# Kernel optimization log

Hardware: AMD Instinct MI355X
Metric: run time of the kernel (lower is better)

The kernel has to match this reference:

```python
import jax, jax.numpy as jnp
import numpy as np

# Gating config (matches init_kwargs)
N_GROUPS = 4        # n_expert_groups
TOPK_GROUPS = 2     # n_limited_groups
TOPK = 4            # n_activated_experts
ROUTE_SCALE = 1.0


def setup_inputs() -> dict:
    key = jax.random.key(0)
    ks = jax.random.split(key, 8)
    T, D, E, I = 2048, 1024, 16, 512
    s = 0.02  # init scale for sane numerics
    return {
        "x": jax.random.normal(ks[0], (T, D), jnp.float32),
        "gate_w": jax.random.normal(ks[1], (E, D), jnp.float32) * s,
        "w1": jax.random.normal(ks[2], (E, I, D), jnp.float32) * s,
        "w2": jax.random.normal(ks[3], (E, D, I), jnp.float32) * s,
        "w3": jax.random.normal(ks[4], (E, I, D), jnp.float32) * s,
        "ws1": jax.random.normal(ks[5], (I, D), jnp.float32) * s,
        "ws2": jax.random.normal(ks[6], (D, I), jnp.float32) * s,
        "ws3": jax.random.normal(ks[7], (I, D), jnp.float32) * s,
    }


def _gate(x, gate_w):
    # GateDeepSeekV3.forward: softmax scores, group-limited routing, top-k experts.
    T = x.shape[0]
    scores = jax.nn.softmax((x @ gate_w.T).astype(jnp.float32), axis=-1)  # [T, E]
    original_scores = scores
    E = scores.shape[-1]
    # group-limited routing: keep top `TOPK_GROUPS` groups by max score (bias is None)
    s = scores.reshape(T, N_GROUPS, E // N_GROUPS)
    group_scores = s.max(axis=-1)                                  # [T, G]
    _, gidx = jax.lax.top_k(group_scores, TOPK_GROUPS)             # [T, Gk]
    mask = jnp.zeros((T, N_GROUPS), scores.dtype).at[jnp.arange(T)[:, None], gidx].set(1.0)
    s = (s * mask[:, :, None]).reshape(T, E)
    _, indices = jax.lax.top_k(s, TOPK)                            # [T, topk]
    weights = jnp.take_along_axis(original_scores, indices, axis=1) * ROUTE_SCALE
    return weights.astype(x.dtype), indices


def reference(x, gate_w, w1, w2, w3, ws1, ws2, ws3):
    T, D = x.shape
    E = w1.shape[0]
    weights, indices = _gate(x, gate_w)
    # dense [T, E] combine weights (topk indices are unique per token)
    gate_dense = jnp.zeros((T, E), x.dtype).at[jnp.arange(T)[:, None], indices].add(weights)
    # routed experts: y_t = sum_e g[t,e] * W2_e (silu(W1_e x) * (W3_e x))
    h = jax.nn.silu(jnp.einsum('td,eid->tei', x, w1)) * jnp.einsum('td,eid->tei', x, w3)
    y = jnp.einsum('tei,te,edi->td', h, gate_dense, w2)
    # shared expert MLP over all tokens
    z = (jax.nn.silu(x @ ws1.T) * (x @ ws3.T)) @ ws2.T
    return y + z
```

## Files before the change

### kernel.cpp

```cpp
#include <hip/hip_runtime.h>
#include <hip/hip_bf16.h>
#include <math.h>

typedef float v4f __attribute__((ext_vector_type(4)));
typedef short v8s __attribute__((ext_vector_type(8)));

#define T_TOK   2048
#define DDIM    1024
#define NE      16
#define IDIM    512
#define S_ROUTED 8192
#define S_ALL   10240
#define MAXTILE 104

#define OFF_TOPKI    0u
#define OFF_TOPKW    32768u
#define OFF_PART     65536u
#define OFF_CBASE    69632u
#define OFF_SEGOFF   73728u
#define OFF_NTILES   74240u
#define OFF_TROW     74752u
#define OFF_TEND     75776u
#define OFF_TEXP     76800u
#define OFF_SLOTWT   81920u
#define OFF_S2T      114688u
#define OFF_SLOTOF   155648u
#define OFF_XBF      (1u<<20)
#define OFF_H        (8u<<20)
#define OFF_YP       (24u<<20)

__device__ __forceinline__ unsigned short f2bf(float f) {
    unsigned int u = __float_as_uint(f);
    unsigned int r = (u + 0x7fffu + ((u >> 16) & 1u)) >> 16;
    return (unsigned short)r;
}
__device__ __forceinline__ float bf2f(unsigned short s) {
    return __uint_as_float((unsigned)s << 16);
}

#define GLL16(gp, lp) __builtin_amdgcn_global_load_lds( \
    (__attribute__((address_space(1))) void*)(gp), \
    (__attribute__((address_space(3))) void*)(lp), 16, 0, 0)

__global__ __launch_bounds__(256) void gate_kernel(
    const float* __restrict__ x, const float* __restrict__ gw,
    int* __restrict__ topki, float* __restrict__ topkw,
    unsigned short* __restrict__ xbf)
{
    int t = blockIdx.x;
    int tid = threadIdx.x, lane = tid & 63, wave = tid >> 6;
    const float4* xr = (const float4*)(x + (size_t)t * DDIM);
    float4 xv[4];
#pragma unroll
    for (int j = 0; j < 4; j++) xv[j] = xr[lane + 64 * j];

    __shared__ float sc[NE];
#pragma unroll
    for (int ee = 0; ee < 4; ee++) {
        int e = wave * 4 + ee;
        const float4* wr = (const float4*)(gw + (size_t)e * DDIM);
        float acc = 0.f;
#pragma unroll
        for (int j = 0; j < 4; j++) {
            float4 w = wr[lane + 64 * j];
            acc += xv[j].x * w.x + xv[j].y * w.y + xv[j].z * w.z + xv[j].w * w.w;
        }
#pragma unroll
        for (int off = 32; off; off >>= 1) acc += __shfl_down(acc, off, 64);
        if (lane == 0) sc[e] = acc;
    }
    if (wave == 0) {
#pragma unroll
        for (int j = 0; j < 4; j++) {
            int base = 4 * (lane + 64 * j);
            uint2 p;
            p.x = (unsigned)f2bf(xv[j].x) | ((unsigned)f2bf(xv[j].y) << 16);
            p.y = (unsigned)f2bf(xv[j].z) | ((unsigned)f2bf(xv[j].w) << 16);
            *(uint2*)(xbf + (size_t)t * DDIM + base) = p;
        }
    }
    __syncthreads();
    if (tid == 0) {
        float mx = sc[0];
#pragma unroll
        for (int e = 1; e < NE; e++) mx = fmaxf(mx, sc[e]);
        float sco[NE]; float sum = 0.f;
#pragma unroll
        for (int e = 0; e < NE; e++) { sco[e] = __expf(sc[e] - mx); sum += sco[e]; }
        float inv = 1.f / sum;
#pragma unroll
        for (int e = 0; e < NE; e++) sco[e] *= inv;
        float gs[4];
#pragma unroll
        for (int g = 0; g < 4; g++) {
            float m = sco[4 * g];
            m = fmaxf(m, sco[4 * g + 1]); m = fmaxf(m, sco[4 * g + 2]); m = fmaxf(m, sco[4 * g + 3]);
            gs[g] = m;
        }
        int g0 = 0;
        for (int g = 1; g < 4; g++) if (gs[g] > gs[g0]) g0 = g;
        int g1 = -1;
        for (int g = 0; g < 4; g++) { if (g == g0) continue; if (g1 < 0 || gs[g] > gs[g1]) g1 = g; }
        float ms[NE];
#pragma unroll
        for (int e = 0; e < NE; e++) {
            int g = e >> 2;
            ms[e] = (g == g0 || g == g1) ? sco[e] : 0.0f;
        }
        bool used[NE] = {false};
        for (int k = 0; k < 4; k++) {
            int best = -1;
            for (int e = 0; e < NE; e++) {
                if (used[e]) continue;
                if (best < 0 || ms[e] > ms[best]) best = e;
            }
            used[best] = true;
            topki[t * 4 + k] = best;
            topkw[t * 4 + k] = sco[best];
        }
    }
}

__global__ __launch_bounds__(256) void hist_kernel(
    const int* __restrict__ topki, int* __restrict__ part)
{
    __shared__ int cnt[16];
    int tid = threadIdx.x, b = blockIdx.x;
    if (tid < 16) cnt[tid] = 0;
    __syncthreads();
    int e = topki[b * 256 + tid];
    int lane = tid & 63;
#pragma unroll
    for (int e0 = 0; e0 < 16; e0++) {
        unsigned long long mask = __ballot(e == e0);
        if (lane == 0) atomicAdd(&cnt[e0], __popcll(mask));
    }
    __syncthreads();
    if (tid < 16) part[b * 16 + tid] = cnt[tid];
}

__global__ __launch_bounds__(256) void scan_kernel(
    const int* __restrict__ part, int* __restrict__ cbase, int* __restrict__ segoff,
    int* __restrict__ trow, int* __restrict__ tend, int* __restrict__ texp,
    int* __restrict__ ntp)
{
    int tid = threadIdx.x;
    __shared__ int tot[16];
    __shared__ int so[17];
    if (tid < 16) {
        int s = 0;
        for (int b = 0; b < 32; b++) s += part[b * 16 + tid];
        tot[tid] = s;
    }
    __syncthreads();
    if (tid == 0) {
        int off = 0;
        for (int e = 0; e < 16; e++) { so[e] = off; segoff[e] = off; off += tot[e]; }
        so[16] = off; segoff[16] = off; segoff[17] = off + T_TOK;
        int nt = 0;
        for (int e = 0; e < 17; e++) {
            int n = (e < 16) ? tot[e] : T_TOK;
            int base = (e < 16) ? so[e] : S_ROUTED;
            for (int m = 0; m < n; m += 128) {
                trow[nt] = base + m; tend[nt] = base + n; texp[nt] = e; nt++;
            }
        }
        *ntp = nt;
    }
    __syncthreads();
    if (tid < 16) {
        int run = so[tid];
        for (int b = 0; b < 32; b++) { cbase[b * 16 + tid] = run; run += part[b * 16 + tid]; }
    }
}

__global__ __launch_bounds__(256) void assign_kernel(
    const int* __restrict__ topki, const float* __restrict__ topkw,
    const int* __restrict__ cbase, int* __restrict__ s2t,
    float* __restrict__ slotwt, int* __restrict__ slotof)
{
    int b = blockIdx.x, tid = threadIdx.x;
    int i = b * 256 + tid;
    int e = topki[i];
    int lane = tid & 63, wave = tid >> 6;
    __shared__ int wcnt[4][16];
    int lrank = 0;
#pragma unroll
    for (int e0 = 0; e0 < 16; e0++) {
        unsigned long long mask = __ballot(e == e0);
        if (e == e0) lrank = __popcll(mask & ((1ull << lane) - 1ull));
        if (lane == 0) wcnt[wave][e0] = __popcll(mask);
    }
    __syncthreads();
    int pre = 0;
    for (int w = 0; w < wave; w++) pre += wcnt[w][e];
    int slot = cbase[b * 16 + e] + pre + lrank;
    int t = i >> 2;
    s2t[slot] = t;
    slotwt[slot] = topkw[i];
    slotof[i] = slot;
    if ((i & 3) == 0) s2t[S_ROUTED + t] = t;
}

__global__ __launch_bounds__(256, 3) void gemm1_kernel(
    const float* __restrict__ w1, const float* __restrict__ w3,
    const float* __restrict__ s1, const float* __restrict__ s3,
    const unsigned short* __restrict__ xbf,
    unsigned short* __restrict__ h, const float* __restrict__ slotwt,
    const int* __restrict__ s2t,
    const int* __restrict__ trow, const int* __restrict__ tend,
    const int* __restrict__ texp, const int* __restrict__ ntp)
{
    int bid = blockIdx.x;
    int tile = bid >> 3, ct = bid & 7;
    if (tile >= *ntp) return;
    int row0 = trow[tile], rend = tend[tile], e = texp[tile];
    int n0 = ct * 64;
    const float* B1 = (e < 16) ? (w1 + (size_t)e * 524288) : s1;
    const float* B3 = (e < 16) ? (w3 + (size_t)e * 524288) : s3;

    __shared__ __align__(16) short As[128 * 64];
    __shared__ __align__(16) short Bs[128 * 64];

    int tid = threadIdx.x;
    int lane = tid & 63, wave = tid >> 6;
    int wm = wave & 1, wn = wave >> 1;
    int mq = lane >> 4, nl = lane & 15;
    int rr = lane >> 3, cbl = (lane & 7) ^ rr;

    int tok[4];
#pragma unroll
    for (int j = 0; j < 4; j++)
        tok[j] = s2t[row0 + wave * 32 + j * 8 + rr];

    const float* bsrc[4];
    int brow[4], bblk[4];
#pragma unroll
    for (int j = 0; j < 4; j++) {
        int u = tid + 256 * j;
        brow[j] = u >> 3; bblk[j] = u & 7;
        int half = brow[j] >> 6;
        const float* base = half ? B3 : B1;
        bsrc[j] = base + (size_t)(n0 + (brow[j] & 63)) * DDIM + bblk[j] * 8;
    }

    v4f acc[4][4];
#pragma unroll
    for (int i = 0; i < 4; i++)
#pragma unroll
        for (int j = 0; j < 4; j++) acc[i][j] = (v4f)0.f;

    float4 br0[4], br1[4];
#pragma unroll
    for (int j = 0; j < 4; j++) {
        br0[j] = *(const float4*)(bsrc[j]);
        br1[j] = *(const float4*)(bsrc[j] + 4);
    }

    for (int ki = 0; ki < 16; ki++) {
        int kc = ki * 64;
        __syncthreads();
#pragma unroll
        for (int j = 0; j < 4; j++)
            GLL16(xbf + (size_t)tok[j] * DDIM + kc + cbl * 8, As + wave * 2048 + j * 512);
#pragma unroll
        for (int j = 0; j < 4; j++) {
            uint4 p;
            p.x = (unsigned)f2bf(br0[j].x) | ((unsigned)f2bf(br0[j].y) << 16);
            p.y = (unsigned)f2bf(br0[j].z) | ((unsigned)f2bf(br0[j].w) << 16);
            p.z = (unsigned)f2bf(br1[j].x) | ((unsigned)f2bf(br1[j].y) << 16);
            p.w = (unsigned)f2bf(br1[j].z) | ((unsigned)f2bf(br1[j].w) << 16);
            *(uint4*)(Bs + brow[j] * 64 + ((bblk[j] ^ (brow[j] & 7)) * 8)) = p;
        }
        __syncthreads();
        if (ki < 15) {
#pragma unroll
            for (int j = 0; j < 4; j++) {
                br0[j] = *(const float4*)(bsrc[j] + kc + 64);
                br1[j] = *(const float4*)(bsrc[j] + kc + 68);
            }
        }
#pragma unroll
        for (int ks = 0; ks < 2; ks++) {
            int kb = ks * 4 + mq;
            v8s a[4], b[4];
#pragma unroll
            for (int mi = 0; mi < 4; mi++) {
                int R = wm * 64 + mi * 16 + nl;
                a[mi] = *(const v8s*)(As + R * 64 + ((kb ^ (nl & 7)) * 8));
            }
#pragma unroll
            for (int ni = 0; ni < 4; ni++) {
                int S = (ni >> 1) * 64 + wn * 32 + (ni & 1) * 16 + nl;
                b[ni] = *(const v8s*)(Bs + S * 64 + ((kb ^ (nl & 7)) * 8));
            }
#pragma unroll
            for (int mi = 0; mi < 4; mi++)
#pragma unroll
                for (int ni = 0; ni < 4; ni++)
                    acc[mi][ni] = __builtin_amdgcn_mfma_f32_16x16x32_bf16(a[mi], b[ni], acc[mi][ni], 0, 0, 0);
        }
    }
#pragma unroll
    for (int mi = 0; mi < 4; mi++) {
#pragma unroll
        for (int r = 0; r < 4; r++) {
            int srow = row0 + wm * 64 + mi * 16 + mq * 4 + r;
            if (srow < rend) {
                float g = (srow < S_ROUTED) ? slotwt[srow] : 1.0f;
#pragma unroll
                for (int ni = 0; ni < 2; ni++) {
                    float p1 = acc[mi][ni][r], p3 = acc[mi][ni + 2][r];
                    float sig = 1.f / (1.f + __expf(-p1));
                    h[(size_t)srow * IDIM + n0 + wn * 32 + ni * 16 + nl] = f2bf(p1 * sig * p3 * g);
                }
            }
        }
    }
}

__global__ __launch_bounds__(256, 3) void gemm2_kernel(
    const float* __restrict__ w2, const float* __restrict__ s2w,
    const unsigned short* __restrict__ h, unsigned short* __restrict__ yp,
    const int* __restrict__ trow, const int* __restrict__ tend,
    const int* __restrict__ texp, const int* __restrict__ ntp)
{
    int bid = blockIdx.x;
    int tile = bid >> 3, ct = bid & 7;
    if (tile >= *ntp) return;
    int row0 = trow[tile], rend = tend[tile], e = texp[tile];
    int n0 = ct * 128;
    const float* B = ((e < 16) ? (w2 + (size_t)e * 524288) : s2w) + (size_t)n0 * IDIM;

    __shared__ __align__(16) short As[128 * 64];
    __shared__ __align__(16) short Bs[128 * 64];

    int tid = threadIdx.x;
    int lane = tid & 63, wave = tid >> 6;
    int wm = wave & 1, wn = wave >> 1;
    int mq = lane >> 4, nl = lane & 15;
    int rr = lane >> 3, cbl = (lane & 7) ^ rr;

    const float* bsrc[4];
    int brow[4], bblk[4];
#pragma unroll
    for (int j = 0; j < 4; j++) {
        int u = tid + 256 * j;
        brow[j] = u >> 3; bblk[j] = u & 7;
        bsrc[j] = B + (size_t)brow[j] * IDIM + bblk[j] * 8;
    }

    v4f acc[4][4];
#pragma unroll
    for (int i = 0; i < 4; i++)
#pragma unroll
        for (int j = 0; j < 4; j++) acc[i][j] = (v4f)0.f;

    float4 br0[4], br1[4];
#pragma unroll
    for (int j = 0; j < 4; j++) {
        br0[j] = *(const float4*)(bsrc[j]);
        br1[j] = *(const float4*)(bsrc[j] + 4);
    }

    for (int ki = 0; ki < 8; ki++) {
        int kc = ki * 64;
        __syncthreads();
#pragma unroll
        for (int j = 0; j < 4; j++)
            GLL16(h + (size_t)(row0 + wave * 32 + j * 8 + rr) * IDIM + kc + cbl * 8,
                  As + wave * 2048 + j * 512);
#pragma unroll
        for (int j = 0; j < 4; j++) {
            uint4 p;
            p.x = (unsigned)f2bf(br0[j].x) | ((unsigned)f2bf(br0[j].y) << 16);
            p.y = (unsigned)f2bf(br0[j].z) | ((unsigned)f2bf(br0[j].w) << 16);
            p.z = (unsigned)f2bf(br1[j].x) | ((unsigned)f2bf(br1[j].y) << 16);
            p.w = (unsigned)f2bf(br1[j].z) | ((unsigned)f2bf(br1[j].w) << 16);
            *(uint4*)(Bs + brow[j] * 64 + ((bblk[j] ^ (brow[j] & 7)) * 8)) = p;
        }
        __syncthreads();
        if (ki < 7) {
#pragma unroll
            for (int j = 0; j < 4; j++) {
                br0[j] = *(const float4*)(bsrc[j] + kc + 64);
                br1[j] = *(const float4*)(bsrc[j] + kc + 68);
            }
        }
#pragma unroll
        for (int ks = 0; ks < 2; ks++) {
            int kb = ks * 4 + mq;
            v8s a[4], b[4];
#pragma unroll
            for (int mi = 0; mi < 4; mi++) {
                int R = wm * 64 + mi * 16 + nl;
                a[mi] = *(const v8s*)(As + R * 64 + ((kb ^ (nl & 7)) * 8));
            }
#pragma unroll
            for (int ni = 0; ni < 4; ni++) {
                int S = wn * 64 + ni * 16 + nl;
                b[ni] = *(const v8s*)(Bs + S * 64 + ((kb ^ (nl & 7)) * 8));
            }
#pragma unroll
            for (int mi = 0; mi < 4; mi++)
#pragma unroll
                for (int ni = 0; ni < 4; ni++)
                    acc[mi][ni] = __builtin_amdgcn_mfma_f32_16x16x32_bf16(a[mi], b[ni], acc[mi][ni], 0, 0, 0);
        }
    }
#pragma unroll
    for (int mi = 0; mi < 4; mi++) {
#pragma unroll
        for (int r = 0; r < 4; r++) {
            int srow = row0 + wm * 64 + mi * 16 + mq * 4 + r;
            if (srow < rend) {
                unsigned short* yrow = yp + ((size_t)srow << 10) + n0 + wn * 64 + nl;
#pragma unroll
                for (int ni = 0; ni < 4; ni++)
                    yrow[ni * 16] = f2bf(acc[mi][ni][r]);
            }
        }
    }
}

__global__ __launch_bounds__(256) void combine_kernel(
    const unsigned short* __restrict__ yp, const int* __restrict__ slotof,
    float* __restrict__ out)
{
    int t = blockIdx.x;
    int c = threadIdx.x * 4;
    int s0 = slotof[t * 4 + 0], s1 = slotof[t * 4 + 1];
    int s2 = slotof[t * 4 + 2], s3 = slotof[t * 4 + 3];
    ushort4 v  = *(const ushort4*)(yp + (((size_t)(S_ROUTED + t)) << 10) + c);
    ushort4 a0 = *(const ushort4*)(yp + (((size_t)s0) << 10) + c);
    ushort4 a1 = *(const ushort4*)(yp + (((size_t)s1) << 10) + c);
    ushort4 a2 = *(const ushort4*)(yp + (((size_t)s2) << 10) + c);
    ushort4 a3 = *(const ushort4*)(yp + (((size_t)s3) << 10) + c);
    float4 o;
    o.x = bf2f(v.x) + bf2f(a0.x) + bf2f(a1.x) + bf2f(a2.x) + bf2f(a3.x);
    o.y = bf2f(v.y) + bf2f(a0.y) + bf2f(a1.y) + bf2f(a2.y) + bf2f(a3.y);
    o.z = bf2f(v.z) + bf2f(a0.z) + bf2f(a1.z) + bf2f(a2.z) + bf2f(a3.z);
    o.w = bf2f(v.w) + bf2f(a0.w) + bf2f(a1.w) + bf2f(a2.w) + bf2f(a3.w);
    *(float4*)(out + (((size_t)t) << 10) + c) = o;
}

extern "C" void kernel_launch(void* const* d_in, const int* in_sizes, int n_in,
                              void* d_out, int out_size, void* d_ws, size_t ws_size,
                              hipStream_t stream) {
    const float* x    = (const float*)d_in[0];
    const float* gw   = (const float*)d_in[1];
    const float* w1   = (const float*)d_in[2];
    const float* w2   = (const float*)d_in[3];
    const float* w3   = (const float*)d_in[4];
    const float* wsh1 = (const float*)d_in[5];
    const float* wsh2 = (const float*)d_in[6];
    const float* wsh3 = (const float*)d_in[7];
    float* out = (float*)d_out;

    char* ws = (char*)d_ws;
    int*   topki  = (int*)(ws + OFF_TOPKI);
    float* topkw  = (float*)(ws + OFF_TOPKW);
    int*   part   = (int*)(ws + OFF_PART);
    int*   cbase  = (int*)(ws + OFF_CBASE);
    int*   segoff = (int*)(ws + OFF_SEGOFF);
    int*   ntp    = (int*)(ws + OFF_NTILES);
    int*   trow   = (int*)(ws + OFF_TROW);
    int*   tend   = (int*)(ws + OFF_TEND);
    int*   texp   = (int*)(ws + OFF_TEXP);
    float* slotwt = (float*)(ws + OFF_SLOTWT);
    int*   s2t    = (int*)(ws + OFF_S2T);
    int*   slotof = (int*)(ws + OFF_SLOTOF);
    unsigned short* xbf = (unsigned short*)(ws + OFF_XBF);
    unsigned short* h   = (unsigned short*)(ws + OFF_H);
    unsigned short* yp  = (unsigned short*)(ws + OFF_YP);

    gate_kernel<<<T_TOK, 256, 0, stream>>>(x, gw, topki, topkw, xbf);
    hist_kernel<<<32, 256, 0, stream>>>(topki, part);
    scan_kernel<<<1, 256, 0, stream>>>(part, cbase, segoff, trow, tend, texp, ntp);
    assign_kernel<<<32, 256, 0, stream>>>(topki, topkw, cbase, s2t, slotwt, slotof);
    gemm1_kernel<<<MAXTILE * 8, 256, 0, stream>>>(w1, w3, wsh1, wsh3, xbf, h, slotwt, s2t,
                                                  trow, tend, texp, ntp);
    gemm2_kernel<<<MAXTILE * 8, 256, 0, stream>>>(w2, wsh2, h, yp, trow, tend, texp, ntp);
    combine_kernel<<<T_TOK, 256, 0, stream>>>(yp, slotof, out);
}
```

Baseline: 227.9 us.

## Double-buffer LDS tiles in both expert GEMM kernels, one barrier per k-step

Both grouped GEMM kernels now keep two LDS buffers for the A and B tiles. The next k-slice is issued as global and direct-to-LDS loads into the spare buffer while MFMAs run on the current one. This cuts the two barriers per iteration to one and hides load latency behind compute. LDS use per block doubles (64 KB), so occupancy drops from 3 to 2 blocks per CU, as the launch bounds now state.

After: 267.8 us. 1.18x slower.

```diff
diff --git a/kernel.cpp b/kernel.cpp
--- a/kernel.cpp
+++ b/kernel.cpp
@@ -202,7 +202,7 @@
     if ((i & 3) == 0) s2t[S_ROUTED + t] = t;
 }
 
-__global__ __launch_bounds__(256, 3) void gemm1_kernel(
+__global__ __launch_bounds__(256, 2) void gemm1_kernel(
     const float* __restrict__ w1, const float* __restrict__ w3,
     const float* __restrict__ s1, const float* __restrict__ s3,
     const unsigned short* __restrict__ xbf,
@@ -219,8 +219,8 @@
     const float* B1 = (e < 16) ? (w1 + (size_t)e * 524288) : s1;
     const float* B3 = (e < 16) ? (w3 + (size_t)e * 524288) : s3;
 
-    __shared__ __align__(16) short As[128 * 64];
-    __shared__ __align__(16) short Bs[128 * 64];
+    __shared__ __align__(16) short As[2][128 * 64];
+    __shared__ __align__(16) short Bs[2][128 * 64];
 
     int tid = threadIdx.x;
     int lane = tid & 63, wave = tid >> 6;
@@ -234,14 +234,15 @@
         tok[j] = s2t[row0 + wave * 32 + j * 8 + rr];
 
     const float* bsrc[4];
-    int brow[4], bblk[4];
+    int boff[4];
 #pragma unroll
     for (int j = 0; j < 4; j++) {
         int u = tid + 256 * j;
-        brow[j] = u >> 3; bblk[j] = u & 7;
-        int half = brow[j] >> 6;
+        int brow = u >> 3, bblk = u & 7;
+        boff[j] = brow * 64 + ((bblk ^ (brow & 7)) * 8);
+        int half = brow >> 6;
         const float* base = half ? B3 : B1;
-        bsrc[j] = base + (size_t)(n0 + (brow[j] & 63)) * DDIM + bblk[j] * 8;
+        bsrc[j] = base + (size_t)(n0 + (brow & 63)) * DDIM + bblk * 8;
     }
 
     v4f acc[4][4];
@@ -256,29 +257,37 @@
         br0[j] = *(const float4*)(bsrc[j]);
         br1[j] = *(const float4*)(bsrc[j] + 4);
     }
-
+#pragma unroll
+    for (int j = 0; j < 4; j++)
+        GLL16(xbf + (size_t)tok[j] * DDIM + cbl * 8, (short*)As[0] + wave * 2048 + j * 512);
+#pragma unroll
+    for (int j = 0; j < 4; j++) {
+        uint4 p;
+        p.x = (unsigned)f2bf(br0[j].x) | ((unsigned)f2bf(br0[j].y) << 16);
+        p.y = (unsigned)f2bf(br0[j].z) | ((unsigned)f2bf(br0[j].w) << 16);
+        p.z = (unsigned)f2bf(br1[j].x) | ((unsigned)f2bf(br1[j].y) << 16);
+        p.w = (unsigned)f2bf(br1[j].z) | ((unsigned)f2bf(br1[j].w) << 16);
+        *(uint4*)((short*)Bs[0] + boff[j]) = p;
+    }
+    __syncthreads();
+
+    int cur = 0;
     for (int ki = 0; ki < 16; ki++) {
-        int kc = ki * 64;
-        __syncthreads();
-#pragma unroll
-        for (int j = 0; j < 4; j++)
-            GLL16(xbf + (size_t)tok[j] * DDIM + kc + cbl * 8, As + wave * 2048 + j * 512);
-#pragma unroll
-        for (int j = 0; j < 4; j++) {
-            uint4 p;
-            p.x = (unsigned)f2bf(br0[j].x) | ((unsigned)f2bf(br0[j].y) << 16);
-            p.y = (unsigned)f2bf(br0[j].z) | ((unsigned)f2bf(br0[j].w) << 16);
-            p.z = (unsigned)f2bf(br1[j].x) | ((unsigned)f2bf(br1[j].y) << 16);
-            p.w = (unsigned)f2bf(br1[j].z) | ((unsigned)f2bf(br1[j].w) << 16);
-            *(uint4*)(Bs + brow[j] * 64 + ((bblk[j] ^ (brow[j] & 7)) * 8)) = p;
-        }
-        __syncthreads();
+        short* Acur = (short*)As[cur];
+        short* Bcur = (short*)Bs[cur];
+        short* Anxt = (short*)As[cur ^ 1];
+        short* Bnxt = (short*)Bs[cur ^ 1];
         if (ki < 15) {
+            int kc = (ki + 1) * 64;
 #pragma unroll
             for (int j = 0; j < 4; j++) {
-                br0[j] = *(const float4*)(bsrc[j] + kc + 64);
-                br1[j] = *(const float4*)(bsrc[j] + kc + 68);
-            }
+                br0[j] = *(const float4*)(bsrc[j] + kc);
+                br1[j] = *(const float4*)(bsrc[j] + kc + 4);
+            }
+#pragma unroll
+            for (int j = 0; j < 4; j++)
+                GLL16(xbf + (size_t)tok[j] * DDIM + kc + cbl * 8,
+                      Anxt + wave * 2048 + j * 512);
         }
 #pragma unroll
         for (int ks = 0; ks < 2; ks++) {
@@ -287,12 +296,12 @@
 #pragma unroll
             for (int mi = 0; mi < 4; mi++) {
                 int R = wm * 64 + mi * 16 + nl;
-                a[mi] = *(const v8s*)(As + R * 64 + ((kb ^ (nl & 7)) * 8));
+                a[mi] = *(const v8s*)(Acur + R * 64 + ((kb ^ (nl & 7)) * 8));
             }
 #pragma unroll
             for (int ni = 0; ni < 4; ni++) {
                 int S = (ni >> 1) * 64 + wn * 32 + (ni & 1) * 16 + nl;
-                b[ni] = *(const v8s*)(Bs + S * 64 + ((kb ^ (nl & 7)) * 8));
+                b[ni] = *(const v8s*)(Bcur + S * 64 + ((kb ^ (nl & 7)) * 8));
             }
 #pragma unroll
             for (int mi = 0; mi < 4; mi++)
@@ -300,6 +309,19 @@
                 for (int ni = 0; ni < 4; ni++)
                     acc[mi][ni] = __builtin_amdgcn_mfma_f32_16x16x32_bf16(a[mi], b[ni], acc[mi][ni], 0, 0, 0);
         }
+        if (ki < 15) {
+#pragma unroll
+            for (int j = 0; j < 4; j++) {
+                uint4 p;
+                p.x = (unsigned)f2bf(br0[j].x) | ((unsigned)f2bf(br0[j].y) << 16);
+                p.y = (unsigned)f2bf(br0[j].z) | ((unsigned)f2bf(br0[j].w) << 16);
+                p.z = (unsigned)f2bf(br1[j].x) | ((unsigned)f2bf(br1[j].y) << 16);
+                p.w = (unsigned)f2bf(br1[j].z) | ((unsigned)f2bf(br1[j].w) << 16);
+                *(uint4*)(Bnxt + boff[j]) = p;
+            }
+        }
+        __syncthreads();
+        cur ^= 1;
     }
 #pragma unroll
     for (int mi = 0; mi < 4; mi++) {
@@ -319,7 +341,7 @@
     }
 }
 
-__global__ __launch_bounds__(256, 3) void gemm2_kernel(
+__global__ __launch_bounds__(256, 2) void gemm2_kernel(
     const float* __restrict__ w2, const float* __restrict__ s2w,
     const unsigned short* __restrict__ h, unsigned short* __restrict__ yp,
     const int* __restrict__ trow, const int* __restrict__ tend,
@@ -332,8 +354,8 @@
     int n0 = ct * 128;
     const float* B = ((e < 16) ? (w2 + (size_t)e * 524288) : s2w) + (size_t)n0 * IDIM;
 
-    __shared__ __align__(16) short As[128 * 64];
-    __shared__ __align__(16) short Bs[128 * 64];
+    __shared__ __align__(16) short As[2][128 * 64];
+    __shared__ __align__(16) short Bs[2][128 * 64];
 
     int tid = threadIdx.x;
     int lane = tid & 63, wave = tid >> 6;
@@ -342,12 +364,13 @@
     int rr = lane >> 3, cbl = (lane & 7) ^ rr;
 
     const float* bsrc[4];
-    int brow[4], bblk[4];
+    int boff[4];
 #pragma unroll
     for (int j = 0; j < 4; j++) {
         int u = tid + 256 * j;
-        brow[j] = u >> 3; bblk[j] = u & 7;
-        bsrc[j] = B + (size_t)brow[j] * IDIM + bblk[j] * 8;
+        int brow = u >> 3, bblk = u & 7;
+        boff[j] = brow * 64 + ((bblk ^ (brow & 7)) * 8);
+        bsrc[j] = B + (size_t)brow * IDIM + bblk * 8;
     }
 
     v4f acc[4][4];
@@ -362,30 +385,38 @@
         br0[j] = *(const float4*)(bsrc[j]);
         br1[j] = *(const float4*)(bsrc[j] + 4);
     }
-
+#pragma unroll
+    for (int j = 0; j < 4; j++)
+        GLL16(h + (size_t)(row0 + wave * 32 + j * 8 + rr) * IDIM + cbl * 8,
+              (short*)As[0] + wave * 2048 + j * 512);
+#pragma unroll
+    for (int j = 0; j < 4; j++) {
+        uint4 p;
+        p.x = (unsigned)f2bf(br0[j].x) | ((unsigned)f2bf(br0[j].y) << 16);
+        p.y = (unsigned)f2bf(br0[j].z) | ((unsigned)f2bf(br0[j].w) << 16);
+        p.z = (unsigned)f2bf(br1[j].x) | ((unsigned)f2bf(br1[j].y) << 16);
+        p.w = (unsigned)f2bf(br1[j].z) | ((unsigned)f2bf(br1[j].w) << 16);
+        *(uint4*)((short*)Bs[0] + boff[j]) = p;
+    }
+    __syncthreads();
+
+    int cur = 0;
     for (int ki = 0; ki < 8; ki++) {
-        int kc = ki * 64;
-        __syncthreads();
-#pragma unroll
-        for (int j = 0; j < 4; j++)
-            GLL16(h + (size_t)(row0 + wave * 32 + j * 8 + rr) * IDIM + kc + cbl * 8,
-                  As + wave * 2048 + j * 512);
-#pragma unroll
-        for (int j = 0; j < 4; j++) {
-            uint4 p;
-            p.x = (unsigned)f2bf(br0[j].x) | ((unsigned)f2bf(br0[j].y) << 16);
-            p.y = (unsigned)f2bf(br0[j].z) | ((unsigned)f2bf(br0[j].w) << 16);
-            p.z = (unsigned)f2bf(br1[j].x) | ((unsigned)f2bf(br1[j].y) << 16);
-            p.w = (unsigned)f2bf(br1[j].z) | ((unsigned)f2bf(br1[j].w) << 16);
-            *(uint4*)(Bs + brow[j] * 64 + ((bblk[j] ^ (brow[j] & 7)) * 8)) = p;
-        }
-        __syncthreads();
+        short* Acur = (short*)As[cur];
+        short* Bcur = (short*)Bs[cur];
+        short* Anxt = (short*)As[cur ^ 1];
+        short* Bnxt = (short*)Bs[cur ^ 1];
         if (ki < 7) {
+            int kc = (ki + 1) * 64;
 #pragma unroll
             for (int j = 0; j < 4; j++) {
-                br0[j] = *(const float4*)(bsrc[j] + kc + 64);
-                br1[j] = *(const float4*)(bsrc[j] + kc + 68);
-            }
+                br0[j] = *(const float4*)(bsrc[j] + kc);
+                br1[j] = *(const float4*)(bsrc[j] + kc + 4);
+            }
+#pragma unroll
+            for (int j = 0; j < 4; j++)
+                GLL16(h + (size_t)(row0 + wave * 32 + j * 8 + rr) * IDIM + kc + cbl * 8,
+                      Anxt + wave * 2048 + j * 512);
         }
 #pragma unroll
         for (int ks = 0; ks < 2; ks++) {
@@ -394,12 +425,12 @@
 #pragma unroll
             for (int mi = 0; mi < 4; mi++) {
                 int R = wm * 64 + mi * 16 + nl;
-                a[mi] = *(const v8s*)(As + R * 64 + ((kb ^ (nl & 7)) * 8));
+                a[mi] = *(const v8s*)(Acur + R * 64 + ((kb ^ (nl & 7)) * 8));
             }
 #pragma unroll
             for (int ni = 0; ni < 4; ni++) {
                 int S = wn * 64 + ni * 16 + nl;
-                b[ni] = *(const v8s*)(Bs + S * 64 + ((kb ^ (nl & 7)) * 8));
+                b[ni] = *(const v8s*)(Bcur + S * 64 + ((kb ^ (nl & 7)) * 8));
             }
 #pragma unroll
             for (int mi = 0; mi < 4; mi++)
@@ -407,6 +438,19 @@
                 for (int ni = 0; ni < 4; ni++)
                     acc[mi][ni] = __builtin_amdgcn_mfma_f32_16x16x32_bf16(a[mi], b[ni], acc[mi][ni], 0, 0, 0);
         }
+        if (ki < 7) {
+#pragma unroll
+            for (int j = 0; j < 4; j++) {
+                uint4 p;
+                p.x = (unsigned)f2bf(br0[j].x) | ((unsigned)f2bf(br0[j].y) << 16);
+                p.y = (unsigned)f2bf(br0[j].z) | ((unsigned)f2bf(br0[j].w) << 16);
+                p.z = (unsigned)f2bf(br1[j].x) | ((unsigned)f2bf(br1[j].y) << 16);
+                p.w = (unsigned)f2bf(br1[j].z) | ((unsigned)f2bf(br1[j].w) << 16);
+                *(uint4*)(Bnxt + boff[j]) = p;
+            }
+        }
+        __syncthreads();
+        cur ^= 1;
     }
 #pragma unroll
     for (int mi = 0; mi < 4; mi++) {
```

## Double-buffer A tiles and prefetch B two stages ahead in MoE GEMMs

Applied to the files above, without the earlier changes.

Both expert GEMM kernels now keep two LDS buffers for the activation tile and prefetch the fp32 weight registers two k-steps ahead. Barriers and vmcnt waits are placed by hand, with scheduling fences around them, so global loads overlap the MFMA work. The bf16 conversion switches from software rounding to the packed v_cvt_pk_bf16_f32 instruction. This doubles LDS for A and adds 32 more VGPRs of prefetch buffers, which may hurt occupancy under the 3-blocks-per-CU launch bound.

Result: slower. 386.9 us (+69.8%).

```diff
diff --git a/kernel.cpp b/kernel.cpp
--- a/kernel.cpp
+++ b/kernel.cpp
@@ -37,10 +37,17 @@
 __device__ __forceinline__ float bf2f(unsigned short s) {
     return __uint_as_float((unsigned)s << 16);
 }
+__device__ __forceinline__ unsigned cvt2(float lo, float hi) {
+    unsigned r;
+    asm("v_cvt_pk_bf16_f32 %0, %1, %2" : "=v"(r) : "v"(lo), "v"(hi));
+    return r;
+}
 
 #define GLL16(gp, lp) __builtin_amdgcn_global_load_lds( \
     (__attribute__((address_space(1))) void*)(gp), \
     (__attribute__((address_space(3))) void*)(lp), 16, 0, 0)
+
+#define SCHED_FENCE() __builtin_amdgcn_sched_barrier(0)
 
 __global__ __launch_bounds__(256) void gate_kernel(
     const float* __restrict__ x, const float* __restrict__ gw,
@@ -202,6 +209,63 @@
     if ((i & 3) == 0) s2t[S_ROUTED + t] = t;
 }
 
+#define G1_STEP(B0, B1, KI, PB, PA, VMSTR) do {                               \
+    _Pragma("unroll")                                                         \
+    for (int j = 0; j < 4; j++) {                                             \
+        uint4 p;                                                              \
+        p.x = cvt2(B0[j].x, B0[j].y);                                         \
+        p.y = cvt2(B0[j].z, B0[j].w);                                         \
+        p.z = cvt2(B1[j].x, B1[j].y);                                         \
+        p.w = cvt2(B1[j].z, B1[j].w);                                         \
+        *(uint4*)(Bs + boff[j]) = p;                                          \
+    }                                                                         \
+    if (PB) {                                                                 \
+        _Pragma("unroll")                                                     \
+        for (int j = 0; j < 4; j++) {                                         \
+            B0[j] = *(const float4*)(bsrc[j] + (KI + 2) * 64);                \
+            B1[j] = *(const float4*)(bsrc[j] + (KI + 2) * 64 + 4);            \
+        }                                                                     \
+    }                                                                         \
+    if (PA) {                                                                 \
+        _Pragma("unroll")                                                     \
+        for (int j = 0; j < 4; j++)                                           \
+            GLL16(asrc[j] + (KI + 1) * 64,                                    \
+                  (short*)As[(KI + 1) & 1] + wave * 2048 + j * 512);          \
+    }                                                                         \
+    SCHED_FENCE();                                                            \
+    asm volatile("s_waitcnt vmcnt(" VMSTR ") lgkmcnt(0)" ::: "memory");       \
+    SCHED_FENCE();                                                            \
+    __builtin_amdgcn_s_barrier();                                             \
+    SCHED_FENCE();                                                            \
+    {                                                                         \
+        const short* Acur = (const short*)As[(KI) & 1];                       \
+        _Pragma("unroll")                                                     \
+        for (int ks = 0; ks < 2; ks++) {                                      \
+            int kb = ks * 4 + mq;                                             \
+            v8s a[4], b[4];                                                   \
+            _Pragma("unroll")                                                 \
+            for (int mi = 0; mi < 4; mi++) {                                  \
+                int R = wm * 64 + mi * 16 + nl;                               \
+                a[mi] = *(const v8s*)(Acur + R * 64 + ((kb ^ (nl & 7)) * 8)); \
+            }                                                                 \
+            _Pragma("unroll")                                                 \
+            for (int ni = 0; ni < 4; ni++) {                                  \
+                int S = (ni >> 1) * 64 + wn * 32 + (ni & 1) * 16 + nl;        \
+                b[ni] = *(const v8s*)(Bs + S * 64 + ((kb ^ (nl & 7)) * 8));   \
+            }                                                                 \
+            _Pragma("unroll")                                                 \
+            for (int mi = 0; mi < 4; mi++)                                    \
+                _Pragma("unroll")                                             \
+                for (int ni = 0; ni < 4; ni++)                                \
+                    acc[mi][ni] = __builtin_amdgcn_mfma_f32_16x16x32_bf16(    \
+                        a[mi], b[ni], acc[mi][ni], 0, 0, 0);                  \
+    }                                                                         \
+    }                                                                         \
+    SCHED_FENCE();                                                            \
+    __builtin_amdgcn_s_barrier();                                             \
+    SCHED_FENCE();                                                            \
+} while (0)
+
 __global__ __launch_bounds__(256, 3) void gemm1_kernel(
     const float* __restrict__ w1, const float* __restrict__ w3,
     const float* __restrict__ s1, const float* __restrict__ s3,
@@ -219,7 +283,7 @@
     const float* B1 = (e < 16) ? (w1 + (size_t)e * 524288) : s1;
     const float* B3 = (e < 16) ? (w3 + (size_t)e * 524288) : s3;
 
-    __shared__ __align__(16) short As[128 * 64];
+    __shared__ __align__(16) short As[2][128 * 64];
     __shared__ __align__(16) short Bs[128 * 64];
 
     int tid = threadIdx.x;
@@ -228,20 +292,21 @@
     int mq = lane >> 4, nl = lane & 15;
     int rr = lane >> 3, cbl = (lane & 7) ^ rr;
 
-    int tok[4];
+    const unsigned short* asrc[4];
 #pragma unroll
     for (int j = 0; j < 4; j++)
-        tok[j] = s2t[row0 + wave * 32 + j * 8 + rr];
+        asrc[j] = xbf + (size_t)s2t[row0 + wave * 32 + j * 8 + rr] * DDIM + cbl * 8;
 
     const float* bsrc[4];
-    int brow[4], bblk[4];
+    int boff[4];
 #pragma unroll
     for (int j = 0; j < 4; j++) {
         int u = tid + 256 * j;
-        brow[j] = u >> 3; bblk[j] = u & 7;
-        int half = brow[j] >> 6;
+        int brow = u >> 3, bblk = u & 7;
+        boff[j] = brow * 64 + ((bblk ^ (brow & 7)) * 8);
+        int half = brow >> 6;
         const float* base = half ? B3 : B1;
-        bsrc[j] = base + (size_t)(n0 + (brow[j] & 63)) * DDIM + bblk[j] * 8;
+        bsrc[j] = base + (size_t)(n0 + (brow & 63)) * DDIM + bblk * 8;
     }
 
     v4f acc[4][4];
@@ -250,57 +315,29 @@
 #pragma unroll
         for (int j = 0; j < 4; j++) acc[i][j] = (v4f)0.f;
 
-    float4 br0[4], br1[4];
+    float4 bA0[4], bA1[4], bB0[4], bB1[4];
 #pragma unroll
     for (int j = 0; j < 4; j++) {
-        br0[j] = *(const float4*)(bsrc[j]);
-        br1[j] = *(const float4*)(bsrc[j] + 4);
-    }
-
-    for (int ki = 0; ki < 16; ki++) {
-        int kc = ki * 64;
-        __syncthreads();
-#pragma unroll
-        for (int j = 0; j < 4; j++)
-            GLL16(xbf + (size_t)tok[j] * DDIM + kc + cbl * 8, As + wave * 2048 + j * 512);
-#pragma unroll
-        for (int j = 0; j < 4; j++) {
-            uint4 p;
-            p.x = (unsigned)f2bf(br0[j].x) | ((unsigned)f2bf(br0[j].y) << 16);
-            p.y = (unsigned)f2bf(br0[j].z) | ((unsigned)f2bf(br0[j].w) << 16);
-            p.z = (unsigned)f2bf(br1[j].x) | ((unsigned)f2bf(br1[j].y) << 16);
-            p.w = (unsigned)f2bf(br1[j].z) | ((unsigned)f2bf(br1[j].w) << 16);
-            *(uint4*)(Bs + brow[j] * 64 + ((bblk[j] ^ (brow[j] & 7)) * 8)) = p;
-        }
-        __syncthreads();
-        if (ki < 15) {
-#pragma unroll
-            for (int j = 0; j < 4; j++) {
-                br0[j] = *(const float4*)(bsrc[j] + kc + 64);
-                br1[j] = *(const float4*)(bsrc[j] + kc + 68);
-            }
-        }
-#pragma unroll
-        for (int ks = 0; ks < 2; ks++) {
-            int kb = ks * 4 + mq;
-            v8s a[4], b[4];
-#pragma unroll
-            for (int mi = 0; mi < 4; mi++) {
-                int R = wm * 64 + mi * 16 + nl;
-                a[mi] = *(const v8s*)(As + R * 64 + ((kb ^ (nl & 7)) * 8));
-            }
-#pragma unroll
-            for (int ni = 0; ni < 4; ni++) {
-                int S = (ni >> 1) * 64 + wn * 32 + (ni & 1) * 16 + nl;
-                b[ni] = *(const v8s*)(Bs + S * 64 + ((kb ^ (nl & 7)) * 8));
-            }
-#pragma unroll
-            for (int mi = 0; mi < 4; mi++)
-#pragma unroll
-                for (int ni = 0; ni < 4; ni++)
-                    acc[mi][ni] = __builtin_amdgcn_mfma_f32_16x16x32_bf16(a[mi], b[ni], acc[mi][ni], 0, 0, 0);
-        }
-    }
+        bA0[j] = *(const float4*)(bsrc[j]);
+        bA1[j] = *(const float4*)(bsrc[j] + 4);
+    }
+#pragma unroll
+    for (int j = 0; j < 4; j++) {
+        bB0[j] = *(const float4*)(bsrc[j] + 64);
+        bB1[j] = *(const float4*)(bsrc[j] + 68);
+    }
+#pragma unroll
+    for (int j = 0; j < 4; j++)
+        GLL16(asrc[j], (short*)As[0] + wave * 2048 + j * 512);
+    SCHED_FENCE();
+
+    for (int ki = 0; ki < 14; ki += 2) {
+        G1_STEP(bA0, bA1, ki, 1, 1, "12");
+        G1_STEP(bB0, bB1, ki + 1, 1, 1, "12");
+    }
+    G1_STEP(bA0, bA1, 14, 0, 1, "4");
+    G1_STEP(bB0, bB1, 15, 0, 0, "0");
+
 #pragma unroll
     for (int mi = 0; mi < 4; mi++) {
 #pragma unroll
@@ -319,6 +356,63 @@
     }
 }
 
+#define G2_STEP(B0, B1, KI, PB, PA, VMSTR) do {                               \
+    _Pragma("unroll")                                                         \
+    for (int j = 0; j < 4; j++) {                                             \
+        uint4 p;                                                              \
+        p.x = cvt2(B0[j].x, B0[j].y);                                         \
+        p.y = cvt2(B0[j].z, B0[j].w);                                         \
+        p.z = cvt2(B1[j].x, B1[j].y);                                         \
+        p.w = cvt2(B1[j].z, B1[j].w);                                         \
+        *(uint4*)(Bs + boff[j]) = p;                                          \
+    }                                                                         \
+    if (PB) {                                                                 \
+        _Pragma("unroll")                                                     \
+        for (int j = 0; j < 4; j++) {                                         \
+            B0[j] = *(const float4*)(bsrc[j] + (KI + 2) * 64);                \
+            B1[j] = *(const float4*)(bsrc[j] + (KI + 2) * 64 + 4);            \
+        }                                                                     \
+    }                                                                         \
+    if (PA) {                                                                 \
+        _Pragma("unroll")                                                     \
+        for (int j = 0; j < 4; j++)                                           \
+            GLL16(asrc[j] + (KI + 1) * 64,                                    \
+                  (short*)As[(KI + 1) & 1] + wave * 2048 + j * 512);          \
+    }                                                                         \
+    SCHED_FENCE();                                                            \
+    asm volatile("s_waitcnt vmcnt(" VMSTR ") lgkmcnt(0)" ::: "memory");       \
+    SCHED_FENCE();                                                            \
+    __builtin_amdgcn_s_barrier();                                             \
+    SCHED_FENCE();                                                            \
+    {                                                                         \
+        const short* Acur = (const short*)As[(KI) & 1];                       \
+        _Pragma("unroll")                                                     \
+        for (int ks = 0; ks < 2; ks++) {                                      \
+            int kb = ks * 4 + mq;                                             \
+            v8s a[4], b[4];                                                   \
+            _Pragma("unroll")                                                 \
+            for (int mi = 0; mi < 4; mi++) {                                  \
+                int R = wm * 64 + mi * 16 + nl;                               \
+                a[mi] = *(const v8s*)(Acur + R * 64 + ((kb ^ (nl & 7)) * 8)); \
+            }                                                                 \
+            _Pragma("unroll")                                                 \
+            for (int ni = 0; ni < 4; ni++) {                                  \
+                int S = wn * 64 + ni * 16 + nl;                               \
+                b[ni] = *(const v8s*)(Bs + S * 64 + ((kb ^ (nl & 7)) * 8));   \
+            }                                                                 \
+            _Pragma("unroll")                                                 \
+            for (int mi = 0; mi < 4; mi++)                                    \
+                _Pragma("unroll")                                             \
+                for (int ni = 0; ni < 4; ni++)                                \
+                    acc[mi][ni] = __builtin_amdgcn_mfma_f32_16x16x32_bf16(    \
+                        a[mi], b[ni], acc[mi][ni], 0, 0, 0);                  \
+    }                                                                         \
+    }                                                                         \
+    SCHED_FENCE();                                                            \
+    __builtin_amdgcn_s_barrier();                                             \
+    SCHED_FENCE();                                                            \
+} while (0)
+
 __global__ __launch_bounds__(256, 3) void gemm2_kernel(
     const float* __restrict__ w2, const float* __restrict__ s2w,
     const unsigned short* __restrict__ h, unsigned short* __restrict__ yp,
@@ -332,7 +426,7 @@
     int n0 = ct * 128;
     const float* B = ((e < 16) ? (w2 + (size_t)e * 524288) : s2w) + (size_t)n0 * IDIM;
 
-    __shared__ __align__(16) short As[128 * 64];
+    __shared__ __align__(16) short As[2][128 * 64];
     __shared__ __align__(16) short Bs[128 * 64];
 
     int tid = threadIdx.x;
@@ -341,13 +435,19 @@
     int mq = lane >> 4, nl = lane & 15;
     int rr = lane >> 3, cbl = (lane & 7) ^ rr;
 
+    const unsigned short* asrc[4];
+#pragma unroll
+    for (int j = 0; j < 4; j++)
+        asrc[j] = h + (size_t)(row0 + wave * 32 + j * 8 + rr) * IDIM + cbl * 8;
+
     const float* bsrc[4];
-    int brow[4], bblk[4];
+    int boff[4];
 #pragma unroll
     for (int j = 0; j < 4; j++) {
         int u = tid + 256 * j;
-        brow[j] = u >> 3; bblk[j] = u & 7;
-        bsrc[j] = B + (size_t)brow[j] * IDIM + bblk[j] * 8;
+        int brow = u >> 3, bblk = u & 7;
+        boff[j] = brow * 64 + ((bblk ^ (brow & 7)) * 8);
+        bsrc[j] = B + (size_t)brow * IDIM + bblk * 8;
     }
 
     v4f acc[4][4];
@@ -356,58 +456,29 @@
 #pragma unroll
         for (int j = 0; j < 4; j++) acc[i][j] = (v4f)0.f;
 
-    float4 br0[4], br1[4];
+    float4 bA0[4], bA1[4], bB0[4], bB1[4];
 #pragma unroll
     for (int j = 0; j < 4; j++) {
-        br0[j] = *(const float4*)(bsrc[j]);
-        br1[j] = *(const float4*)(bsrc[j] + 4);
-    }
-
-    for (int ki = 0; ki < 8; ki++) {
-        int kc = ki * 64;
-        __syncthreads();
-#pragma unroll
-        for (int j = 0; j < 4; j++)
-            GLL16(h + (size_t)(row0 + wave * 32 + j * 8 + rr) * IDIM + kc + cbl * 8,
-                  As + wave * 2048 + j * 512);
-#pragma unroll
-        for (int j = 0; j < 4; j++) {
-            uint4 p;
-            p.x = (unsigned)f2bf(br0[j].x) | ((unsigned)f2bf(br0[j].y) << 16);
-            p.y = (unsigned)f2bf(br0[j].z) | ((unsigned)f2bf(br0[j].w) << 16);
-            p.z = (unsigned)f2bf(br1[j].x) | ((unsigned)f2bf(br1[j].y) << 16);
-            p.w = (unsigned)f2bf(br1[j].z) | ((unsigned)f2bf(br1[j].w) << 16);
-            *(uint4*)(Bs + brow[j] * 64 + ((bblk[j] ^ (brow[j] & 7)) * 8)) = p;
-        }
-        __syncthreads();
-        if (ki < 7) {
-#pragma unroll
-            for (int j = 0; j < 4; j++) {
-                br0[j] = *(const float4*)(bsrc[j] + kc + 64);
-                br1[j] = *(const float4*)(bsrc[j] + kc + 68);
-            }
-        }
-#pragma unroll
-        for (int ks = 0; ks < 2; ks++) {
-            int kb = ks * 4 + mq;
-            v8s a[4], b[4];
-#pragma unroll
-            for (int mi = 0; mi < 4; mi++) {
-                int R = wm * 64 + mi * 16 + nl;
-                a[mi] = *(const v8s*)(As + R * 64 + ((kb ^ (nl & 7)) * 8));
-            }
-#pragma unroll
-            for (int ni = 0; ni < 4; ni++) {
-                int S = wn * 64 + ni * 16 + nl;
-                b[ni] = *(const v8s*)(Bs + S * 64 + ((kb ^ (nl & 7)) * 8));
-            }
-#pragma unroll
-            for (int mi = 0; mi < 4; mi++)
-#pragma unroll
-                for (int ni = 0; ni < 4; ni++)
-                    acc[mi][ni] = __builtin_amdgcn_mfma_f32_16x16x32_bf16(a[mi], b[ni], acc[mi][ni], 0, 0, 0);
-        }
-    }
+        bA0[j] = *(const float4*)(bsrc[j]);
+        bA1[j] = *(const float4*)(bsrc[j] + 4);
+    }
+#pragma unroll
+    for (int j = 0; j < 4; j++) {
+        bB0[j] = *(const float4*)(bsrc[j] + 64);
+        bB1[j] = *(const float4*)(bsrc[j] + 68);
+    }
+#pragma unroll
+    for (int j = 0; j < 4; j++)
+        GLL16(asrc[j], (short*)As[0] + wave * 2048 + j * 512);
+    SCHED_FENCE();
+
+    for (int ki = 0; ki < 6; ki += 2) {
+        G2_STEP(bA0, bA1, ki, 1, 1, "12");
+        G2_STEP(bB0, bB1, ki + 1, 1, 1, "12");
+    }
+    G2_STEP(bA0, bA1, 6, 0, 1, "4");
+    G2_STEP(bB0, bB1, 7, 0, 0, "0");
+
 #pragma unroll
     for (int mi = 0; mi < 4; mi++) {
 #pragma unroll
```

## Register-prefetch A tiles and use hardware packed bf16 conversion in GEMMs

Applied to the files above, without the earlier changes.

Both expert GEMM kernels stop using direct global-to-LDS loads for the activation tile. Instead they prefetch the next A tile into registers alongside the B prefetch, so the load overlaps the MFMA work of the current step. The hand-written round-to-nearest bf16 packing is replaced by the packed v_cvt_pk_bf16_f32 instruction, and swizzled LDS offsets are precomputed. The min-occupancy hint of 3 blocks is dropped from launch bounds, trading occupancy guarantees for extra register room that the prefetch buffers need.

Measured after the change: 305.0 us. 33.8% more time.

```diff
diff --git a/kernel.cpp b/kernel.cpp
--- a/kernel.cpp
+++ b/kernel.cpp
@@ -37,10 +37,11 @@
 __device__ __forceinline__ float bf2f(unsigned short s) {
     return __uint_as_float((unsigned)s << 16);
 }
-
-#define GLL16(gp, lp) __builtin_amdgcn_global_load_lds( \
-    (__attribute__((address_space(1))) void*)(gp), \
-    (__attribute__((address_space(3))) void*)(lp), 16, 0, 0)
+__device__ __forceinline__ unsigned cvt2(float lo, float hi) {
+    unsigned r;
+    asm("v_cvt_pk_bf16_f32 %0, %1, %2" : "=v"(r) : "v"(lo), "v"(hi));
+    return r;
+}
 
 __global__ __launch_bounds__(256) void gate_kernel(
     const float* __restrict__ x, const float* __restrict__ gw,
@@ -202,7 +203,7 @@
     if ((i & 3) == 0) s2t[S_ROUTED + t] = t;
 }
 
-__global__ __launch_bounds__(256, 3) void gemm1_kernel(
+__global__ __launch_bounds__(256) void gemm1_kernel(
     const float* __restrict__ w1, const float* __restrict__ w3,
     const float* __restrict__ s1, const float* __restrict__ s3,
     const unsigned short* __restrict__ xbf,
@@ -228,20 +229,21 @@
     int mq = lane >> 4, nl = lane & 15;
     int rr = lane >> 3, cbl = (lane & 7) ^ rr;
 
-    int tok[4];
+    const unsigned short* asrc[4];
 #pragma unroll
     for (int j = 0; j < 4; j++)
-        tok[j] = s2t[row0 + wave * 32 + j * 8 + rr];
+        asrc[j] = xbf + (size_t)s2t[row0 + wave * 32 + j * 8 + rr] * DDIM + cbl * 8;
 
     const float* bsrc[4];
-    int brow[4], bblk[4];
+    int boff[4];
 #pragma unroll
     for (int j = 0; j < 4; j++) {
         int u = tid + 256 * j;
-        brow[j] = u >> 3; bblk[j] = u & 7;
-        int half = brow[j] >> 6;
+        int brow = u >> 3, bblk = u & 7;
+        boff[j] = brow * 64 + ((bblk ^ (brow & 7)) * 8);
+        int half = brow >> 6;
         const float* base = half ? B3 : B1;
-        bsrc[j] = base + (size_t)(n0 + (brow[j] & 63)) * DDIM + bblk[j] * 8;
+        bsrc[j] = base + (size_t)(n0 + (brow & 63)) * DDIM + bblk * 8;
     }
 
     v4f acc[4][4];
@@ -250,7 +252,10 @@
 #pragma unroll
         for (int j = 0; j < 4; j++) acc[i][j] = (v4f)0.f;
 
+    uint4 ar[4];
     float4 br0[4], br1[4];
+#pragma unroll
+    for (int j = 0; j < 4; j++) ar[j] = *(const uint4*)(asrc[j]);
 #pragma unroll
     for (int j = 0; j < 4; j++) {
         br0[j] = *(const float4*)(bsrc[j]);
@@ -258,26 +263,28 @@
     }
 
     for (int ki = 0; ki < 16; ki++) {
-        int kc = ki * 64;
         __syncthreads();
 #pragma unroll
         for (int j = 0; j < 4; j++)
-            GLL16(xbf + (size_t)tok[j] * DDIM + kc + cbl * 8, As + wave * 2048 + j * 512);
+            *(uint4*)(As + wave * 2048 + j * 512 + lane * 8) = ar[j];
 #pragma unroll
         for (int j = 0; j < 4; j++) {
             uint4 p;
-            p.x = (unsigned)f2bf(br0[j].x) | ((unsigned)f2bf(br0[j].y) << 16);
-            p.y = (unsigned)f2bf(br0[j].z) | ((unsigned)f2bf(br0[j].w) << 16);
-            p.z = (unsigned)f2bf(br1[j].x) | ((unsigned)f2bf(br1[j].y) << 16);
-            p.w = (unsigned)f2bf(br1[j].z) | ((unsigned)f2bf(br1[j].w) << 16);
-            *(uint4*)(Bs + brow[j] * 64 + ((bblk[j] ^ (brow[j] & 7)) * 8)) = p;
+            p.x = cvt2(br0[j].x, br0[j].y);
+            p.y = cvt2(br0[j].z, br0[j].w);
+            p.z = cvt2(br1[j].x, br1[j].y);
+            p.w = cvt2(br1[j].z, br1[j].w);
+            *(uint4*)(Bs + boff[j]) = p;
         }
         __syncthreads();
         if (ki < 15) {
+            int kc = (ki + 1) * 64;
+#pragma unroll
+            for (int j = 0; j < 4; j++) ar[j] = *(const uint4*)(asrc[j] + kc);
 #pragma unroll
             for (int j = 0; j < 4; j++) {
-                br0[j] = *(const float4*)(bsrc[j] + kc + 64);
-                br1[j] = *(const float4*)(bsrc[j] + kc + 68);
+                br0[j] = *(const float4*)(bsrc[j] + kc);
+                br1[j] = *(const float4*)(bsrc[j] + kc + 4);
             }
         }
 #pragma unroll
@@ -319,7 +326,7 @@
     }
 }
 
-__global__ __launch_bounds__(256, 3) void gemm2_kernel(
+__global__ __launch_bounds__(256) void gemm2_kernel(
     const float* __restrict__ w2, const float* __restrict__ s2w,
     const unsigned short* __restrict__ h, unsigned short* __restrict__ yp,
     const int* __restrict__ trow, const int* __restrict__ tend,
@@ -341,13 +348,19 @@
     int mq = lane >> 4, nl = lane & 15;
     int rr = lane >> 3, cbl = (lane & 7) ^ rr;
 
+    const unsigned short* asrc[4];
+#pragma unroll
+    for (int j = 0; j < 4; j++)
+        asrc[j] = h + (size_t)(row0 + wave * 32 + j * 8 + rr) * IDIM + cbl * 8;
+
     const float* bsrc[4];
-    int brow[4], bblk[4];
+    int boff[4];
 #pragma unroll
     for (int j = 0; j < 4; j++) {
         int u = tid + 256 * j;
-        brow[j] = u >> 3; bblk[j] = u & 7;
-        bsrc[j] = B + (size_t)brow[j] * IDIM + bblk[j] * 8;
+        int brow = u >> 3, bblk = u & 7;
+        boff[j] = brow * 64 + ((bblk ^ (brow & 7)) * 8);
+        bsrc[j] = B + (size_t)brow * IDIM + bblk * 8;
     }
 
     v4f acc[4][4];
@@ -356,7 +369,10 @@
 #pragma unroll
         for (int j = 0; j < 4; j++) acc[i][j] = (v4f)0.f;
 
+    uint4 ar[4];
     float4 br0[4], br1[4];
+#pragma unroll
+    for (int j = 0; j < 4; j++) ar[j] = *(const uint4*)(asrc[j]);
 #pragma unroll
     for (int j = 0; j < 4; j++) {
         br0[j] = *(const float4*)(bsrc[j]);
@@ -364,27 +380,28 @@
     }
 
     for (int ki = 0; ki < 8; ki++) {
-        int kc = ki * 64;
         __syncthreads();
 #pragma unroll
         for (int j = 0; j < 4; j++)
-            GLL16(h + (size_t)(row0 + wave * 32 + j * 8 + rr) * IDIM + kc + cbl * 8,
-                  As + wave * 2048 + j * 512);
+            *(uint4*)(As + wave * 2048 + j * 512 + lane * 8) = ar[j];
 #pragma unroll
         for (int j = 0; j < 4; j++) {
             uint4 p;
-            p.x = (unsigned)f2bf(br0[j].x) | ((unsigned)f2bf(br0[j].y) << 16);
-            p.y = (unsigned)f2bf(br0[j].z) | ((unsigned)f2bf(br0[j].w) << 16);
-            p.z = (unsigned)f2bf(br1[j].x) | ((unsigned)f2bf(br1[j].y) << 16);
-            p.w = (unsigned)f2bf(br1[j].z) | ((unsigned)f2bf(br1[j].w) << 16);
-            *(uint4*)(Bs + brow[j] * 64 + ((bblk[j] ^ (brow[j] & 7)) * 8)) = p;
+            p.x = cvt2(br0[j].x, br0[j].y);
+            p.y = cvt2(br0[j].z, br0[j].w);
+            p.z = cvt2(br1[j].x, br1[j].y);
+            p.w = cvt2(br1[j].z, br1[j].w);
+            *(uint4*)(Bs + boff[j]) = p;
         }
         __syncthreads();
         if (ki < 7) {
+            int kc = (ki + 1) * 64;
+#pragma unroll
+            for (int j = 0; j < 4; j++) ar[j] = *(const uint4*)(asrc[j] + kc);
 #pragma unroll
             for (int j = 0; j < 4; j++) {
-                br0[j] = *(const float4*)(bsrc[j] + kc + 64);
-                br1[j] = *(const float4*)(bsrc[j] + kc + 68);
+                br0[j] = *(const float4*)(bsrc[j] + kc);
+                br1[j] = *(const float4*)(bsrc[j] + kc + 4);
             }
         }
 #pragma unroll
```
